# Optimization experiments

Hardware: AMD Instinct MI355X
Metric: run time of the kernel (lower is better)

Reference implementation:

```python
import jax, jax.numpy as jnp
import numpy as np

B, S, D = 8, 1024, 1024
H, DK = 16, 64  # num_heads, d_k; H*DK == D
NEG_INF = 1e29


def setup_inputs() -> dict:
    key = jax.random.key(0)
    ks = jax.random.split(key, 12)
    sc = 1.0 / np.sqrt(D)
    q = jax.random.normal(ks[0], (B, S, D), jnp.float32)
    k = jax.random.normal(ks[1], (B, S, D), jnp.float32)
    v = jax.random.normal(ks[2], (B, S, D), jnp.float32)
    # causal mask, broadcast per batch (mask==0 positions are masked out)
    mask = jnp.broadcast_to(jnp.tril(jnp.ones((S, S), jnp.int32)), (B, S, S))
    Wq = jax.random.normal(ks[3], (D, D), jnp.float32) * sc
    bq = jax.random.normal(ks[4], (D,), jnp.float32) * 0.01
    Wk = jax.random.normal(ks[5], (D, D), jnp.float32) * sc
    bk = jax.random.normal(ks[6], (D,), jnp.float32) * 0.01
    Wv = jax.random.normal(ks[7], (D, D), jnp.float32) * sc
    bv = jax.random.normal(ks[8], (D,), jnp.float32) * 0.01
    Wo = jax.random.normal(ks[9], (D, D), jnp.float32) * sc
    bo = jax.random.normal(ks[10], (D,), jnp.float32) * 0.01
    return {"q": q, "k": k, "v": v, "mask": mask,
            "Wq": Wq, "bq": bq, "Wk": Wk, "bk": bk,
            "Wv": Wv, "bv": bv, "Wo": Wo, "bo": bo}


def reference(q, k, v, mask, Wq, bq, Wk, bk, Wv, bv, Wo, bo):
    # Linear projections (torch Linear: x @ W.T + b)
    q1 = q @ Wq.T + bq
    k1 = k @ Wk.T + bk
    v1 = v @ Wv.T + bv
    # [B, S, D] -> [B, H, S, DK]
    def split_heads(x):
        return x.reshape(B, S, H, DK).transpose(0, 2, 1, 3)
    q3, k3, v3 = split_heads(q1), split_heads(k1), split_heads(v1)
    # scores [B, H, S, S]
    scores = jnp.einsum('bhqd,bhkd->bhqk', q3, k3) / jnp.sqrt(jnp.float32(DK))
    scores = jnp.where(mask[:, None, :, :] == 0, -NEG_INF, scores)
    probs = jax.nn.softmax(scores, axis=-1)
    attn = jnp.einsum('bhqk,bhkd->bhqd', probs, v3)  # [B, H, S, DK]
    out = attn.transpose(0, 2, 1, 3).reshape(B, S, D)
    return out @ Wo.T + bo
```

## Files before the change

kernel.cpp:

```cpp
#include <hip/hip_runtime.h>
#include <hip/hip_bf16.h>
#include <stdint.h>

constexpr int NB = 8;
constexpr int NS = 1024;
constexpr int ND = 1024;
constexpr int NH = 16;
constexpr int NDK = 64;
constexpr int NKT = ND / 64;

typedef __bf16 bf16_t;
typedef __attribute__((ext_vector_type(8))) __bf16 bf16x8;
typedef __attribute__((ext_vector_type(4))) __bf16 bf16x4;
typedef __attribute__((ext_vector_type(4))) float f32x4;

#define GLL16(g, s) __builtin_amdgcn_global_load_lds( \
    (const __attribute__((address_space(1))) void*)(g), \
    (__attribute__((address_space(3))) void*)(s), 16, 0, 0)

__device__ __forceinline__ void cvt_body(const float* __restrict__ s,
                                         bf16_t* __restrict__ d, long n) {
  long i0 = (long)(blockIdx.x * blockDim.x + threadIdx.x) * 4;
  long step = (long)gridDim.x * blockDim.x * 4;
  for (long i = i0; i < n; i += step) {
    float4 f = *(const float4*)(s + i);
    bf16x4 o;
    o[0] = (bf16_t)f.x; o[1] = (bf16_t)f.y; o[2] = (bf16_t)f.z; o[3] = (bf16_t)f.w;
    *(bf16x4*)(d + i) = o;
  }
}

__global__ __launch_bounds__(256) void cvt4_kernel(const float* s0, bf16_t* d0,
                                                   const float* s1, bf16_t* d1,
                                                   const float* s2, bf16_t* d2,
                                                   const float* s3, bf16_t* d3, long n) {
  const float* s = blockIdx.y == 0 ? s0 : blockIdx.y == 1 ? s1 : blockIdx.y == 2 ? s2 : s3;
  bf16_t* d = blockIdx.y == 0 ? d0 : blockIdx.y == 1 ? d1 : blockIdx.y == 2 ? d2 : d3;
  cvt_body(s, d, n);
}

__global__ __launch_bounds__(512, 2) void gemm_qkv(
    const float* A0, const bf16_t* W0, const float* b0, bf16_t* C0,
    const float* A1, const bf16_t* W1, const float* b1, bf16_t* C1,
    const float* A2, const bf16_t* W2, const float* b2, bf16_t* C2) {
  __shared__ bf16_t S[2 * 16384 + 3 * 8192];
  const int o = blockIdx.x;
  const int xcd = o & 7, s = o >> 3;
  const int bx = s & 7, u = s >> 3;
  const int zby = xcd + 8 * u;
  const int z = zby >> 5, by = zby & 31;
  const float* A = z == 0 ? A0 : z == 1 ? A1 : A2;
  const bf16_t* W = z == 0 ? W0 : z == 1 ? W1 : W2;
  const float* bb = z == 0 ? b0 : z == 1 ? b1 : b2;
  bf16_t* C = z == 0 ? C0 : z == 1 ? C1 : C2;

  const int tid = threadIdx.x;
  const int l = tid & 63, w = tid >> 6;
  const int wr = w >> 1, wc = w & 1;
  const int g = l >> 4, r = l & 15;
  const int m0 = by * 256, n0 = bx * 128;
  const int wbase = w * 512;

  bf16_t* Ab = S;
  bf16_t* Bb = S + 32768;

  float4 faA[8], faB[8];
  auto issueA = [&](int t, float4 (&dst)[8]) {
#pragma unroll
    for (int it = 0; it < 4; ++it) {
      const float* p = A + (size_t)(m0 + it * 64 + (tid >> 3)) * ND + t * 64 + (tid & 7) * 8;
      dst[it * 2]     = *(const float4*)p;
      dst[it * 2 + 1] = *(const float4*)(p + 4);
    }
  };
  auto writeA = [&](int ab, float4 (&src)[8]) {
#pragma unroll
    for (int it = 0; it < 4; ++it) {
      int row = it * 64 + (tid >> 3), c = tid & 7;
      bf16x8 ov;
      ov[0] = (bf16_t)src[it * 2].x;     ov[1] = (bf16_t)src[it * 2].y;
      ov[2] = (bf16_t)src[it * 2].z;     ov[3] = (bf16_t)src[it * 2].w;
      ov[4] = (bf16_t)src[it * 2 + 1].x; ov[5] = (bf16_t)src[it * 2 + 1].y;
      ov[6] = (bf16_t)src[it * 2 + 1].z; ov[7] = (bf16_t)src[it * 2 + 1].w;
      *(bf16x8*)(Ab + ab * 16384 + row * 64 + ((c ^ (row & 7)) << 3)) = ov;
    }
  };
  auto stageB = [&](int qb, int t) {
#pragma unroll
    for (int it = 0; it < 2; ++it) {
      int idx = it * 512 + tid;
      int row = idx >> 3, c = (idx & 7) ^ (row & 7);
      GLL16(W + (size_t)(n0 + row) * ND + (t << 6) + c * 8,
            Bb + qb * 8192 + it * 4096 + wbase);
    }
  };

  f32x4 acc[4][4] = {};

  issueA(0, faA);
  issueA(1, faB);
  stageB(0, 0);
  stageB(1, 1);
  asm volatile("s_waitcnt vmcnt(2)" ::: "memory");
  __builtin_amdgcn_sched_barrier(0);
  writeA(0, faA);
  asm volatile("s_waitcnt lgkmcnt(0)" ::: "memory");
  __builtin_amdgcn_s_barrier();

  auto bodyT = [&](int t, float4 (&fiss)[8], float4 (&fwr)[8]) {
    if (t + 2 < NKT) issueA(t + 2, fiss);
    __builtin_amdgcn_sched_barrier(0);
    if (t + 2 < NKT) stageB((t + 2) % 3, t + 2);
    __builtin_amdgcn_sched_barrier(0);

    const bf16_t* a_ = Ab + (t & 1) * 16384;
    const bf16_t* b_ = Bb + (t % 3) * 8192;
#pragma unroll
    for (int kk = 0; kk < 2; ++kk) {
      bf16x8 af[4], bw[4];
#pragma unroll
      for (int m = 0; m < 4; ++m) {
        int row = wr * 64 + m * 16 + r;
        af[m] = *(const bf16x8*)(a_ + row * 64 + (((kk * 4 + g) ^ (row & 7)) << 3));
      }
#pragma unroll
      for (int n = 0; n < 4; ++n) {
        int row = wc * 64 + n * 16 + r;
        bw[n] = *(const bf16x8*)(b_ + row * 64 + (((kk * 4 + g) ^ (row & 7)) << 3));
      }
      __builtin_amdgcn_s_setprio(1);
#pragma unroll
      for (int m = 0; m < 4; ++m)
#pragma unroll
        for (int n = 0; n < 4; ++n)
          acc[m][n] = __builtin_amdgcn_mfma_f32_16x16x32_bf16(af[m], bw[n], acc[m][n], 0, 0, 0);
      __builtin_amdgcn_s_setprio(0);
    }

    if (t + 2 < NKT)      asm volatile("s_waitcnt vmcnt(10)" ::: "memory");
    else                  asm volatile("s_waitcnt vmcnt(0)" ::: "memory");
    __builtin_amdgcn_sched_barrier(0);
    if (t + 1 < NKT) writeA((t + 1) & 1, fwr);
    asm volatile("s_waitcnt lgkmcnt(0)" ::: "memory");
    __builtin_amdgcn_s_barrier();
  };

#pragma unroll 1
  for (int tt = 0; tt < NKT; tt += 2) {
    bodyT(tt, faA, faB);
    bodyT(tt + 1, faB, faA);
  }

  if (z == 2) {
#pragma unroll
    for (int n = 0; n < 4; ++n) {
      int col = n0 + wc * 64 + n * 16 + r;
      int hh = col >> 6, dk = col & 63;
      float bv = bb[col];
#pragma unroll
      for (int m = 0; m < 4; ++m) {
        int row0 = m0 + wr * 64 + m * 16 + g * 4;
        int b_ = row0 >> 10, s0 = row0 & 1023;
        bf16x4 o4;
#pragma unroll
        for (int j = 0; j < 4; ++j) o4[j] = (bf16_t)(acc[m][n][j] + bv);
        *(bf16x4*)(C + (((size_t)b_ * 16 + hh) * 64 + dk) * 1024 + s0) = o4;
      }
    }
  } else {
#pragma unroll
    for (int n = 0; n < 4; ++n) {
      int col = n0 + wc * 64 + n * 16 + r;
      float bv = bb[col];
#pragma unroll
      for (int m = 0; m < 4; ++m) {
        int row0 = m0 + wr * 64 + m * 16 + g * 4;
#pragma unroll
        for (int j = 0; j < 4; ++j)
          C[(size_t)(row0 + j) * ND + col] = (bf16_t)(acc[m][n][j] + bv);
      }
    }
  }
}

__global__ __launch_bounds__(512, 2) void gemm_bt(const bf16_t* __restrict__ A,
                                                  const bf16_t* __restrict__ W,
                                                  const float* __restrict__ bias,
                                                  float* __restrict__ Cout,
                                                  int M, int N, int K) {
  __shared__ bf16_t S[3 * 24576];
  const int o = blockIdx.x;
  const int xcd = o & 7, s = o >> 3;
  const int bx = s & 7, u = s >> 3;
  const int by = xcd + 8 * u;

  const int tid = threadIdx.x;
  const int l = tid & 63, w = tid >> 6;
  const int wr = w >> 1, wc = w & 1;
  const int g = l >> 4, r = l & 15;
  const int m0 = by * 256, n0 = bx * 128;
  const int wbase = w * 512;

  auto stageA2 = [&](int q, int t, int half) {
#pragma unroll
    for (int it = half * 2; it < half * 2 + 2; ++it) {
      int idx = it * 512 + tid;
      int row = idx >> 3, c = (idx & 7) ^ (row & 7);
      GLL16(A + (size_t)(m0 + row) * K + (t << 6) + c * 8,
            S + q * 24576 + it * 4096 + wbase);
    }
  };
  auto stageB2 = [&](int q, int t) {
#pragma unroll
    for (int it = 0; it < 2; ++it) {
      int idx = it * 512 + tid;
      int row = idx >> 3, c = (idx & 7) ^ (row & 7);
      GLL16(W + (size_t)(n0 + row) * K + (t << 6) + c * 8,
            S + q * 24576 + 16384 + it * 4096 + wbase);
    }
  };

  f32x4 acc[4][4] = {};
  const int NKT2 = K >> 6;

  stageA2(0, 0, 0); stageA2(0, 0, 1); stageB2(0, 0);
  stageA2(1, 1, 0); stageA2(1, 1, 1); stageB2(1, 1);

  int q = 0;
  for (int t = 0; t < NKT2; ++t) {
    const bool pf = (t + 2 < NKT2);
    int q2 = q + 2; if (q2 >= 3) q2 -= 3;

    if (t + 1 < NKT2) asm volatile("s_waitcnt vmcnt(6)" ::: "memory");
    else              asm volatile("s_waitcnt vmcnt(0)" ::: "memory");
    __builtin_amdgcn_s_barrier();

    const bf16_t* a_ = S + q * 24576;
    const bf16_t* b_ = a_ + 16384;

#pragma unroll
    for (int kk = 0; kk < 2; ++kk) {
      bf16x8 bw[4];
#pragma unroll
      for (int n = 0; n < 4; ++n) {
        int row = wc * 64 + n * 16 + r;
        bw[n] = *(const bf16x8*)(b_ + row * 64 + (((kk * 4 + g) ^ (row & 7)) << 3));
      }
#pragma unroll
      for (int mh = 0; mh < 2; ++mh) {
        bf16x8 af[2];
#pragma unroll
        for (int i = 0; i < 2; ++i) {
          int row = wr * 64 + (mh * 2 + i) * 16 + r;
          af[i] = *(const bf16x8*)(a_ + row * 64 + (((kk * 4 + g) ^ (row & 7)) << 3));
        }
        if (pf) {
          int ph = kk * 2 + mh;
          if (ph == 0)      stageA2(q2, t + 2, 0);
          else if (ph == 1) stageA2(q2, t + 2, 1);
          else if (ph == 2) stageB2(q2, t + 2);
        }
        __builtin_amdgcn_s_barrier();
        asm volatile("s_waitcnt lgkmcnt(0)" ::: "memory");
        __builtin_amdgcn_sched_barrier(0);
        __builtin_amdgcn_s_setprio(1);
#pragma unroll
        for (int i = 0; i < 2; ++i)
#pragma unroll
          for (int n = 0; n < 4; ++n)
            acc[mh * 2 + i][n] = __builtin_amdgcn_mfma_f32_16x16x32_bf16(
                af[i], bw[n], acc[mh * 2 + i][n], 0, 0, 0);
        __builtin_amdgcn_s_setprio(0);
        __builtin_amdgcn_sched_barrier(0);
      }
    }
    ++q; if (q >= 3) q -= 3;
  }

#pragma unroll
  for (int n = 0; n < 4; ++n) {
    int col = n0 + wc * 64 + n * 16 + r;
    float bv = bias[col];
#pragma unroll
    for (int m = 0; m < 4; ++m) {
      int row0 = m0 + wr * 64 + m * 16 + g * 4;
#pragma unroll
      for (int j = 0; j < 4; ++j)
        Cout[(size_t)(row0 + j) * N + col] = acc[m][n][j] + bv;
    }
  }
}

__global__ __launch_bounds__(512, 4) void attn_kernel(const bf16_t* __restrict__ Q1,
                                                      const bf16_t* __restrict__ K1,
                                                      const bf16_t* __restrict__ V1t,
                                                      bf16_t* __restrict__ attn) {
  __shared__ bf16_t Kt[2][64 * 64];
  __shared__ bf16_t Vt[2][64 * 64];
  __shared__ bf16_t Pl[8][16 * 64];

  const int tid = threadIdx.x;
  const int l = tid & 63, w = tid >> 6;
  const int g = l >> 4, r = l & 15;

  const int o = blockIdx.x;
  const int os = (o & 7) * 64 + (o >> 3);
  const int pair = os & 3, hb = os >> 2;
  const int h = hb & 15, b = hb >> 4;

  constexpr float SC = 0.18033688011112042f;
  const bf16_t* vbase = V1t + ((size_t)(b * 16 + h) * 64) * 1024;

  auto stageKV = [&](int kt2, int pb) {
    const int k0 = kt2 * 64;
    int row = tid >> 3;
    int c = (tid & 7) ^ (row & 7);
    GLL16(K1 + ((size_t)b * NS + k0 + row) * ND + h * 64 + c * 8,
          &Kt[pb][w * 512]);
    GLL16(vbase + (size_t)row * 1024 + k0 + c * 8,
          &Vt[pb][w * 512]);
  };

  for (int ph = 0; ph < 2; ++ph) {
    const int qt = ph ? (7 - pair) : pair;
    const int qrow_g = qt * 128 + w * 16 + r;

    const bf16_t* qptr = Q1 + ((size_t)b * NS + qrow_g) * ND + h * 64;
    bf16x8 qf0 = *(const bf16x8*)(qptr + g * 8);
    bf16x8 qf1 = *(const bf16x8*)(qptr + 32 + g * 8);
#pragma unroll
    for (int i = 0; i < 8; ++i) {
      qf0[i] = (bf16_t)((float)qf0[i] * SC);
      qf1[i] = (bf16_t)((float)qf1[i] * SC);
    }

    float mrun = -1e30f, lrun = 0.f;
    f32x4 oacc[4] = {};

    __syncthreads();

    const int nkt = 2 * qt + 2;
    stageKV(0, 0);

    for (int kt = 0; kt < nkt; ++kt) {
      const int p = kt & 1;
      const int k0 = kt * 64;

      __syncthreads();

      if (kt + 1 < nkt) stageKV(kt + 1, p ^ 1);

      f32x4 sacc[4] = {};
      __builtin_amdgcn_s_setprio(1);
#pragma unroll
      for (int n = 0; n < 4; ++n) {
        int key = n * 16 + r;
#pragma unroll
        for (int kk = 0; kk < 2; ++kk) {
          int dk2 = kk * 32 + g * 8;
          int boff = key * 128 + ((dk2 * 2) ^ ((key & 7) << 4));
          bf16x8 kf = *(const bf16x8*)((char*)Kt[p] + boff);
          sacc[n] = __builtin_amdgcn_mfma_f32_16x16x32_bf16(kf, kk == 0 ? qf0 : qf1, sacc[n], 0, 0, 0);
        }
      }
      __builtin_amdgcn_s_setprio(0);

      if (kt >= 2 * qt) {
#pragma unroll
        for (int n = 0; n < 4; ++n)
#pragma unroll
          for (int j = 0; j < 4; ++j)
            if (k0 + n * 16 + g * 4 + j > qrow_g) sacc[n][j] = -1e30f;
      }

      float mx;
      {
        float t0 = fmaxf(fmaxf(sacc[0][0], sacc[0][1]), fmaxf(sacc[0][2], sacc[0][3]));
        float t1 = fmaxf(fmaxf(sacc[1][0], sacc[1][1]), fmaxf(sacc[1][2], sacc[1][3]));
        float t2 = fmaxf(fmaxf(sacc[2][0], sacc[2][1]), fmaxf(sacc[2][2], sacc[2][3]));
        float t3 = fmaxf(fmaxf(sacc[3][0], sacc[3][1]), fmaxf(sacc[3][2], sacc[3][3]));
        mx = fmaxf(fmaxf(t0, t1), fmaxf(t2, t3));
      }
      mx = fmaxf(mx, __shfl_xor(mx, 16));
      mx = fmaxf(mx, __shfl_xor(mx, 32));

      if (!__all(mx <= mrun + 8.0f)) {
        float m_new = fmaxf(mrun, mx);
        float esc = __builtin_amdgcn_exp2f(mrun - m_new);
        mrun = m_new;
        lrun *= esc;
#pragma unroll
        for (int n = 0; n < 4; ++n)
#pragma unroll
          for (int j = 0; j < 4; ++j) oacc[n][j] *= esc;
      }

      float rsum = 0.f;
#pragma unroll
      for (int n = 0; n < 4; ++n) {
        bf16x4 p4;
#pragma unroll
        for (int j = 0; j < 4; ++j) {
          float pe = __builtin_amdgcn_exp2f(sacc[n][j] - mrun);
          rsum += pe;
          p4[j] = (bf16_t)pe;
        }
        *(bf16x4*)((char*)Pl[w] + r * 128 + ((n * 32 + g * 8) ^ ((r & 7) << 4))) = p4;
      }
      rsum += __shfl_xor(rsum, 16);
      rsum += __shfl_xor(rsum, 32);
      lrun += rsum;

      __builtin_amdgcn_s_setprio(1);
#pragma unroll
      for (int kk = 0; kk < 2; ++kk) {
        bf16x8 pf = *(const bf16x8*)((char*)Pl[w] + r * 128 + ((kk * 64 + g * 16) ^ ((r & 7) << 4)));
#pragma unroll
        for (int n = 0; n < 4; ++n) {
          int dkr = n * 16 + r;
          bf16x8 vf = *(const bf16x8*)((char*)Vt[p] + dkr * 128 + ((kk * 64 + g * 16) ^ ((dkr & 7) << 4)));
          oacc[n] = __builtin_amdgcn_mfma_f32_16x16x32_bf16(vf, pf, oacc[n], 0, 0, 0);
        }
      }
      __builtin_amdgcn_s_setprio(0);
    }

    float linv = 1.0f / lrun;
#pragma unroll
    for (int n = 0; n < 4; ++n) {
      bf16x4 o4;
#pragma unroll
      for (int j = 0; j < 4; ++j) o4[j] = (bf16_t)(oacc[n][j] * linv);
      *(bf16x4*)(attn + ((size_t)b * NS + qrow_g) * ND + h * 64 + n * 16 + g * 4) = o4;
    }
  }
}

extern "C" void kernel_launch(void* const* d_in, const int* in_sizes, int n_in,
                              void* d_out, int out_size, void* d_ws, size_t ws_size,
                              hipStream_t stream) {
  const float* q  = (const float*)d_in[0];
  const float* k  = (const float*)d_in[1];
  const float* v  = (const float*)d_in[2];
  const float* Wq = (const float*)d_in[4];
  const float* bq = (const float*)d_in[5];
  const float* Wk = (const float*)d_in[6];
  const float* bk = (const float*)d_in[7];
  const float* Wv = (const float*)d_in[8];
  const float* bv = (const float*)d_in[9];
  const float* Wo = (const float*)d_in[10];
  const float* bo = (const float*)d_in[11];
  float* out = (float*)d_out;

  const size_t NX = (size_t)NB * NS * ND;
  const size_t NW = (size_t)ND * ND;
  char* ws = (char*)d_ws;
  size_t off = 0;
  auto alloc = [&](size_t bytes) {
    char* p = ws + off;
    off += (bytes + 255) & ~(size_t)255;
    return p;
  };
  bf16_t* wqb = (bf16_t*)alloc(NW * 2);
  bf16_t* wkb = (bf16_t*)alloc(NW * 2);
  bf16_t* wvb = (bf16_t*)alloc(NW * 2);
  bf16_t* wob = (bf16_t*)alloc(NW * 2);
  bf16_t* q1  = (bf16_t*)alloc(NX * 2);
  bf16_t* k1  = (bf16_t*)alloc(NX * 2);
  bf16_t* v1t = (bf16_t*)alloc(NX * 2);
  bf16_t* at  = (bf16_t*)alloc(NX * 2);

  dim3 blk(256);
  cvt4_kernel<<<dim3(128, 4), blk, 0, stream>>>(Wq, wqb, Wk, wkb, Wv, wvb, Wo, wob, (long)NW);

  gemm_qkv<<<dim3(768), dim3(512), 0, stream>>>(
      q, wqb, bq, q1, k, wkb, bk, k1, v, wvb, bv, v1t);

  attn_kernel<<<dim3(512), dim3(512), 0, stream>>>(q1, k1, v1t, at);

  gemm_bt<<<dim3(256), dim3(512), 0, stream>>>(at, wob, bo, out, NB * NS, ND, ND);
}
```

Before: 144.4 us.

## Switch attention to 32x32x16 MFMA with register-resident P via permlane32 swap

Reworks the attention kernel so each wave handles 32 query rows using 32x32x16 bf16 MFMAs instead of 16x16x32, with 256-thread blocks. The softmax probabilities stay in registers: they are packed with v_cvt_pk_bf16_f32 and rearranged with v_permlane32_swap, which removes the per-wave LDS round trip for P. This targets LDS traffic and instruction overhead in the attention inner loop. In exchange, each wave holds more accumulator registers, and a block now has half as many threads to cover the staging loads.

```diff
diff --git a/kernel.cpp b/kernel.cpp
--- a/kernel.cpp
+++ b/kernel.cpp
@@ -13,10 +13,17 @@
 typedef __attribute__((ext_vector_type(8))) __bf16 bf16x8;
 typedef __attribute__((ext_vector_type(4))) __bf16 bf16x4;
 typedef __attribute__((ext_vector_type(4))) float f32x4;
+typedef __attribute__((ext_vector_type(16))) float f32x16;
 
 #define GLL16(g, s) __builtin_amdgcn_global_load_lds( \
     (const __attribute__((address_space(1))) void*)(g), \
     (__attribute__((address_space(3))) void*)(s), 16, 0, 0)
+
+__device__ __forceinline__ unsigned cvtpk_bf16(float lo, float hi) {
+  unsigned r;
+  asm("v_cvt_pk_bf16_f32 %0, %1, %2" : "=v"(r) : "v"(lo), "v"(hi));
+  return r;
+}
 
 __device__ __forceinline__ void cvt_body(const float* __restrict__ s,
                                          bf16_t* __restrict__ d, long n) {
@@ -291,17 +298,16 @@
   }
 }
 
-__global__ __launch_bounds__(512, 4) void attn_kernel(const bf16_t* __restrict__ Q1,
+__global__ __launch_bounds__(256, 2) void attn_kernel(const bf16_t* __restrict__ Q1,
                                                       const bf16_t* __restrict__ K1,
                                                       const bf16_t* __restrict__ V1t,
                                                       bf16_t* __restrict__ attn) {
   __shared__ bf16_t Kt[2][64 * 64];
   __shared__ bf16_t Vt[2][64 * 64];
-  __shared__ bf16_t Pl[8][16 * 64];
 
   const int tid = threadIdx.x;
   const int l = tid & 63, w = tid >> 6;
-  const int g = l >> 4, r = l & 15;
+  const int q32 = l & 31, h5 = l >> 5;
 
   const int o = blockIdx.x;
   const int os = (o & 7) * 64 + (o >> 3);
@@ -313,29 +319,32 @@
 
   auto stageKV = [&](int kt2, int pb) {
     const int k0 = kt2 * 64;
-    int row = tid >> 3;
-    int c = (tid & 7) ^ (row & 7);
-    GLL16(K1 + ((size_t)b * NS + k0 + row) * ND + h * 64 + c * 8,
-          &Kt[pb][w * 512]);
-    GLL16(vbase + (size_t)row * 1024 + k0 + c * 8,
-          &Vt[pb][w * 512]);
+#pragma unroll
+    for (int it = 0; it < 2; ++it) {
+      int idx = it * 256 + tid;
+      int row = idx >> 3, c = (idx & 7) ^ (row & 7);
+      GLL16(K1 + ((size_t)b * NS + k0 + row) * ND + h * 64 + c * 8,
+            &Kt[pb][it * 2048 + w * 512]);
+      GLL16(vbase + (size_t)row * 1024 + k0 + c * 8,
+            &Vt[pb][it * 2048 + w * 512]);
+    }
   };
 
   for (int ph = 0; ph < 2; ++ph) {
     const int qt = ph ? (7 - pair) : pair;
-    const int qrow_g = qt * 128 + w * 16 + r;
+    const int qrow_g = qt * 128 + w * 32 + q32;
 
     const bf16_t* qptr = Q1 + ((size_t)b * NS + qrow_g) * ND + h * 64;
-    bf16x8 qf0 = *(const bf16x8*)(qptr + g * 8);
-    bf16x8 qf1 = *(const bf16x8*)(qptr + 32 + g * 8);
-#pragma unroll
-    for (int i = 0; i < 8; ++i) {
-      qf0[i] = (bf16_t)((float)qf0[i] * SC);
-      qf1[i] = (bf16_t)((float)qf1[i] * SC);
+    bf16x8 qf[4];
+#pragma unroll
+    for (int ds = 0; ds < 4; ++ds) {
+      qf[ds] = *(const bf16x8*)(qptr + ds * 16 + h5 * 8);
+#pragma unroll
+      for (int i = 0; i < 8; ++i) qf[ds][i] = (bf16_t)((float)qf[ds][i] * SC);
     }
 
     float mrun = -1e30f, lrun = 0.f;
-    f32x4 oacc[4] = {};
+    f32x16 oacc0 = {}, oacc1 = {};
 
     __syncthreads();
 
@@ -350,38 +359,38 @@
 
       if (kt + 1 < nkt) stageKV(kt + 1, p ^ 1);
 
-      f32x4 sacc[4] = {};
+      f32x16 s0 = {}, s1 = {};
       __builtin_amdgcn_s_setprio(1);
 #pragma unroll
-      for (int n = 0; n < 4; ++n) {
-        int key = n * 16 + r;
-#pragma unroll
-        for (int kk = 0; kk < 2; ++kk) {
-          int dk2 = kk * 32 + g * 8;
-          int boff = key * 128 + ((dk2 * 2) ^ ((key & 7) << 4));
-          bf16x8 kf = *(const bf16x8*)((char*)Kt[p] + boff);
-          sacc[n] = __builtin_amdgcn_mfma_f32_16x16x32_bf16(kf, kk == 0 ? qf0 : qf1, sacc[n], 0, 0, 0);
+      for (int ds = 0; ds < 4; ++ds) {
+        int dk2b = (ds * 16 + h5 * 8) * 2;
+        {
+          int row = q32;
+          bf16x8 kf = *(const bf16x8*)((char*)Kt[p] + row * 128 + (dk2b ^ ((row & 7) << 4)));
+          s0 = __builtin_amdgcn_mfma_f32_32x32x16_bf16(kf, qf[ds], s0, 0, 0, 0);
+        }
+        {
+          int row = 32 + q32;
+          bf16x8 kf = *(const bf16x8*)((char*)Kt[p] + row * 128 + (dk2b ^ ((row & 7) << 4)));
+          s1 = __builtin_amdgcn_mfma_f32_32x32x16_bf16(kf, qf[ds], s1, 0, 0, 0);
         }
       }
       __builtin_amdgcn_s_setprio(0);
 
       if (kt >= 2 * qt) {
 #pragma unroll
-        for (int n = 0; n < 4; ++n)
-#pragma unroll
-          for (int j = 0; j < 4; ++j)
-            if (k0 + n * 16 + g * 4 + j > qrow_g) sacc[n][j] = -1e30f;
-      }
-
-      float mx;
-      {
-        float t0 = fmaxf(fmaxf(sacc[0][0], sacc[0][1]), fmaxf(sacc[0][2], sacc[0][3]));
-        float t1 = fmaxf(fmaxf(sacc[1][0], sacc[1][1]), fmaxf(sacc[1][2], sacc[1][3]));
-        float t2 = fmaxf(fmaxf(sacc[2][0], sacc[2][1]), fmaxf(sacc[2][2], sacc[2][3]));
-        float t3 = fmaxf(fmaxf(sacc[3][0], sacc[3][1]), fmaxf(sacc[3][2], sacc[3][3]));
-        mx = fmaxf(fmaxf(t0, t1), fmaxf(t2, t3));
-      }
-      mx = fmaxf(mx, __shfl_xor(mx, 16));
+        for (int reg = 0; reg < 16; ++reg) {
+          int key = k0 + (reg & 3) + 8 * (reg >> 2) + 4 * h5;
+          if (key > qrow_g) s0[reg] = -1e30f;
+          if (key + 32 > qrow_g) s1[reg] = -1e30f;
+        }
+      }
+
+      float mx = s0[0];
+#pragma unroll
+      for (int i = 1; i < 16; ++i) mx = fmaxf(mx, s0[i]);
+#pragma unroll
+      for (int i = 0; i < 16; ++i) mx = fmaxf(mx, s1[i]);
       mx = fmaxf(mx, __shfl_xor(mx, 32));
 
       if (!__all(mx <= mrun + 8.0f)) {
@@ -390,48 +399,70 @@
         mrun = m_new;
         lrun *= esc;
 #pragma unroll
-        for (int n = 0; n < 4; ++n)
-#pragma unroll
-          for (int j = 0; j < 4; ++j) oacc[n][j] *= esc;
+        for (int i = 0; i < 16; ++i) { oacc0[i] *= esc; oacc1[i] *= esc; }
       }
 
       float rsum = 0.f;
 #pragma unroll
-      for (int n = 0; n < 4; ++n) {
-        bf16x4 p4;
-#pragma unroll
-        for (int j = 0; j < 4; ++j) {
-          float pe = __builtin_amdgcn_exp2f(sacc[n][j] - mrun);
-          rsum += pe;
-          p4[j] = (bf16_t)pe;
-        }
-        *(bf16x4*)((char*)Pl[w] + r * 128 + ((n * 32 + g * 8) ^ ((r & 7) << 4))) = p4;
-      }
-      rsum += __shfl_xor(rsum, 16);
+      for (int i = 0; i < 16; ++i) { s0[i] = __builtin_amdgcn_exp2f(s0[i] - mrun); rsum += s0[i]; }
+#pragma unroll
+      for (int i = 0; i < 16; ++i) { s1[i] = __builtin_amdgcn_exp2f(s1[i] - mrun); rsum += s1[i]; }
       rsum += __shfl_xor(rsum, 32);
       lrun += rsum;
 
+      bf16x8 pf[4];
+#pragma unroll
+      for (int ks = 0; ks < 4; ++ks) {
+        const int base = (ks & 1) * 8;
+        unsigned ca, cb, cc, cd;
+        if (ks < 2) {
+          ca = cvtpk_bf16(s0[base + 0], s0[base + 1]);
+          cb = cvtpk_bf16(s0[base + 2], s0[base + 3]);
+          cc = cvtpk_bf16(s0[base + 4], s0[base + 5]);
+          cd = cvtpk_bf16(s0[base + 6], s0[base + 7]);
+        } else {
+          ca = cvtpk_bf16(s1[base + 0], s1[base + 1]);
+          cb = cvtpk_bf16(s1[base + 2], s1[base + 3]);
+          cc = cvtpk_bf16(s1[base + 4], s1[base + 5]);
+          cd = cvtpk_bf16(s1[base + 6], s1[base + 7]);
+        }
+        asm volatile("v_permlane32_swap_b32 %0, %1" : "+v"(ca), "+v"(cc));
+        asm volatile("v_permlane32_swap_b32 %0, %1" : "+v"(cb), "+v"(cd));
+        union { unsigned u[4]; bf16x8 v; } pw;
+        pw.u[0] = ca; pw.u[1] = cb; pw.u[2] = cc; pw.u[3] = cd;
+        pf[ks] = pw.v;
+      }
+
       __builtin_amdgcn_s_setprio(1);
 #pragma unroll
-      for (int kk = 0; kk < 2; ++kk) {
-        bf16x8 pf = *(const bf16x8*)((char*)Pl[w] + r * 128 + ((kk * 64 + g * 16) ^ ((r & 7) << 4)));
-#pragma unroll
-        for (int n = 0; n < 4; ++n) {
-          int dkr = n * 16 + r;
-          bf16x8 vf = *(const bf16x8*)((char*)Vt[p] + dkr * 128 + ((kk * 64 + g * 16) ^ ((dkr & 7) << 4)));
-          oacc[n] = __builtin_amdgcn_mfma_f32_16x16x32_bf16(vf, pf, oacc[n], 0, 0, 0);
+      for (int ks = 0; ks < 4; ++ks) {
+        int key2b = (ks * 16 + h5 * 8) * 2;
+        {
+          int row = q32;
+          bf16x8 vf = *(const bf16x8*)((char*)Vt[p] + row * 128 + (key2b ^ ((row & 7) << 4)));
+          oacc0 = __builtin_amdgcn_mfma_f32_32x32x16_bf16(vf, pf[ks], oacc0, 0, 0, 0);
+        }
+        {
+          int row = 32 + q32;
+          bf16x8 vf = *(const bf16x8*)((char*)Vt[p] + row * 128 + (key2b ^ ((row & 7) << 4)));
+          oacc1 = __builtin_amdgcn_mfma_f32_32x32x16_bf16(vf, pf[ks], oacc1, 0, 0, 0);
         }
       }
       __builtin_amdgcn_s_setprio(0);
     }
 
     float linv = 1.0f / lrun;
-#pragma unroll
-    for (int n = 0; n < 4; ++n) {
-      bf16x4 o4;
-#pragma unroll
-      for (int j = 0; j < 4; ++j) o4[j] = (bf16_t)(oacc[n][j] * linv);
-      *(bf16x4*)(attn + ((size_t)b * NS + qrow_g) * ND + h * 64 + n * 16 + g * 4) = o4;
+    bf16_t* optr = attn + ((size_t)b * NS + qrow_g) * ND + h * 64;
+#pragma unroll
+    for (int rr = 0; rr < 4; ++rr) {
+      bf16x4 o4a, o4b;
+#pragma unroll
+      for (int j = 0; j < 4; ++j) {
+        o4a[j] = (bf16_t)(oacc0[rr * 4 + j] * linv);
+        o4b[j] = (bf16_t)(oacc1[rr * 4 + j] * linv);
+      }
+      *(bf16x4*)(optr + rr * 8 + h5 * 4) = o4a;
+      *(bf16x4*)(optr + 32 + rr * 8 + h5 * 4) = o4b;
     }
   }
 }
@@ -476,7 +507,7 @@
   gemm_qkv<<<dim3(768), dim3(512), 0, stream>>>(
       q, wqb, bq, q1, k, wkb, bk, k1, v, wvb, bv, v1t);
 
-  attn_kernel<<<dim3(512), dim3(512), 0, stream>>>(q1, k1, v1t, at);
+  attn_kernel<<<dim3(512), dim3(256), 0, stream>>>(q1, k1, v1t, at);
 
   gemm_bt<<<dim3(256), dim3(512), 0, stream>>>(at, wob, bo, out, NB * NS, ND, ND);
 }
```

Result: no change. 144.2 us (-0.1%).
